# Optimization experiments

Measured on AMD Instinct MI355X. Metric: run time of the kernel, lower is better.

## Reference

```python
import jax, jax.numpy as jnp
import numpy as np

N = 50000          # nodes
E = 800000         # edges
IN = 256           # input feature dim
HID = 64           # hidden per-head dim
OUT = 64           # output dim
H1, H2 = 4, 1      # heads per layer
NEG_SLOPE = 0.2    # DGL GATConv default


def setup_inputs() -> dict:
    key = jax.random.key(0)
    ks = jax.random.split(key, 12)
    features = jax.random.normal(ks[0], (N, IN), dtype=jnp.float32)
    src = jax.random.randint(ks[1], (E,), 0, N, dtype=jnp.int32)
    dst = jax.random.randint(ks[2], (E,), 0, N, dtype=jnp.int32)
    s1 = 1.0 / np.sqrt(IN)
    s2 = 1.0 / np.sqrt(HID * H1)
    W1 = jax.random.normal(ks[3], (IN, H1 * HID), dtype=jnp.float32) * s1
    al1 = jax.random.normal(ks[4], (H1, HID), dtype=jnp.float32) * 0.1
    ar1 = jax.random.normal(ks[5], (H1, HID), dtype=jnp.float32) * 0.1
    b1 = jnp.zeros((H1, HID), dtype=jnp.float32)
    W2 = jax.random.normal(ks[6], (H1 * HID, H2 * OUT), dtype=jnp.float32) * s2
    al2 = jax.random.normal(ks[7], (H2, OUT), dtype=jnp.float32) * 0.1
    ar2 = jax.random.normal(ks[8], (H2, OUT), dtype=jnp.float32) * 0.1
    b2 = jnp.zeros((H2, OUT), dtype=jnp.float32)
    return {"features": features, "src": src, "dst": dst,
            "W1": W1, "al1": al1, "ar1": ar1, "b1": b1,
            "W2": W2, "al2": al2, "ar2": ar2, "b2": b2}


def gat_layer(h, src, dst, W, al, ar, b, heads, out_dim, activate):
    # projection: (N, H, D)
    feat = (h @ W).reshape(N, heads, out_dim)
    # per-node attention halves: (N, H)
    el = jnp.einsum('nhd,hd->nh', feat, al)
    er = jnp.einsum('nhd,hd->nh', feat, ar)
    # edge logits with leaky relu: (E, H)
    e = el[src] + er[dst]
    e = jnp.where(e >= 0, e, NEG_SLOPE * e)
    # edge softmax grouped by destination node
    emax = jax.ops.segment_max(e, dst, num_segments=N)      # (N, H)
    ee = jnp.exp(e - emax[dst])
    esum = jax.ops.segment_sum(ee, dst, num_segments=N)     # (N, H)
    alpha = ee / esum[dst]                                  # (E, H)
    # weighted scatter-sum of source features: (N, H, D)
    msg = alpha[:, :, None] * feat[src]
    out = jax.ops.segment_sum(msg, dst, num_segments=N) + b[None]
    if activate:
        out = jax.nn.relu(out)
    return out


def reference(features, src, dst, W1, al1, ar1, b1, W2, al2, ar2, b2):
    h = gat_layer(features, src, dst, W1, al1, ar1, b1, H1, HID, True)
    h = h.reshape(N, H1 * HID)                 # flatten(1)
    h = gat_layer(h, src, dst, W2, al2, ar2, b2, H2, OUT, False)
    return h.mean(axis=1)                      # mean over heads -> (N, OUT)
```

## Files before the change

### kernel.cpp

```cpp
#include <hip/hip_runtime.h>
#include <hip/hip_fp16.h>

#define NN   50000
#define NE   800000
#define IND  256
#define HIDD 64
#define OUTD 64
#define NH1  4
#define NH2  1
#define NEG  0.2f

#define NBUK 196
#define NCHK 256
#define CE   3125
#define MAXDEG 96

typedef float f32x4 __attribute__((ext_vector_type(4)));
typedef short s16x8 __attribute__((ext_vector_type(8)));

__device__ __forceinline__ short bf16_rne(float f) {
    unsigned u = __float_as_uint(f);
    unsigned r = u + 0x7FFFu + ((u >> 16) & 1u);
    return (short)(r >> 16);
}

__global__ void cnt1a_k(const int* __restrict__ key, int* __restrict__ cnt,
                        const float* __restrict__ W1, const float* __restrict__ W2,
                        short* __restrict__ Wt1, short* __restrict__ Wt2) {
    __shared__ int lc[NBUK];
    int tid = threadIdx.x, chunk = blockIdx.x;
    for (int idx = chunk * 256 + tid; idx < IND * IND + IND * OUTD; idx += NCHK * 256) {
        if (idx < IND * IND) {
            int k = idx / IND, n = idx - k * IND;
            Wt1[(size_t)n * IND + k] = bf16_rne(W1[idx]);
        } else {
            int i2 = idx - IND * IND;
            int k = i2 / OUTD, n = i2 - k * OUTD;
            Wt2[(size_t)n * IND + k] = bf16_rne(W2[i2]);
        }
    }
    for (int j = tid; j < NBUK; j += 256) lc[j] = 0;
    __syncthreads();
    const int* kc = key + (size_t)chunk * CE;
    for (int t = tid; t < CE; t += 256) atomicAdd(&lc[kc[t] >> 8], 1);
    __syncthreads();
    for (int j = tid; j < NBUK; j += 256) cnt[j * NCHK + chunk] = lc[j];
}

__global__ void cnt1b_k(const unsigned* __restrict__ ein, int* __restrict__ cnt) {
    __shared__ int lc[NBUK];
    int tid = threadIdx.x, chunk = blockIdx.x;
    for (int j = tid; j < NBUK; j += 256) lc[j] = 0;
    __syncthreads();
    const unsigned* ec = ein + (size_t)chunk * CE;
    for (int t = tid; t < CE; t += 256) atomicAdd(&lc[(ec[t] & 0xFFFFu) >> 8], 1);
    __syncthreads();
    for (int j = tid; j < NBUK; j += 256) cnt[j * NCHK + chunk] = lc[j];
}

__global__ void scanC_k(int* __restrict__ cnt, int* __restrict__ buktot) {
    int b    = blockIdx.x * 4 + (threadIdx.x >> 6);
    int lane = threadIdx.x & 63;
    if (b >= NBUK) return;
    int base = b * NCHK + lane * 4;
    int4 v = *(int4*)&cnt[base];
    int s0 = v.x, s1 = s0 + v.y, s2 = s1 + v.z, s3 = s2 + v.w;
    int inc = s3;
    for (int o = 1; o < 64; o <<= 1) {
        int t = __shfl_up(inc, o);
        if (lane >= o) inc += t;
    }
    int excl = inc - s3;
    int4 w;
    w.x = excl; w.y = excl + s0; w.z = excl + s1; w.w = excl + s2;
    *(int4*)&cnt[base] = w;
    if (lane == 63) buktot[b] = inc;
}

__global__ void fill1a_k(const int* __restrict__ src, const int* __restrict__ dst,
                         const int* __restrict__ cnt, const int* __restrict__ buktot,
                         unsigned* __restrict__ eout) {
    __shared__ int cur[NBUK];
    __shared__ int tmp[256];
    int tid = threadIdx.x, chunk = blockIdx.x;
    int v = (tid < NBUK) ? buktot[tid] : 0;
    tmp[tid] = v;
    __syncthreads();
    for (int o = 1; o < 256; o <<= 1) {
        int add = (tid >= o) ? tmp[tid - o] : 0;
        __syncthreads();
        tmp[tid] += add;
        __syncthreads();
    }
    if (tid < NBUK) cur[tid] = cnt[tid * NCHK + chunk] + tmp[tid] - v;
    __syncthreads();
    size_t base = (size_t)chunk * CE;
    for (int t = tid; t < CE; t += 256) {
        int s = src[base + t], d = dst[base + t];
        int pos = atomicAdd(&cur[s >> 8], 1);
        eout[pos] = ((unsigned)s << 16) | (unsigned)d;
    }
}

__global__ void fill1b_k(const unsigned* __restrict__ ein, const int* __restrict__ cnt,
                         const int* __restrict__ buktot, unsigned* __restrict__ eout) {
    __shared__ int cur[NBUK];
    __shared__ int tmp[256];
    int tid = threadIdx.x, chunk = blockIdx.x;
    int v = (tid < NBUK) ? buktot[tid] : 0;
    tmp[tid] = v;
    __syncthreads();
    for (int o = 1; o < 256; o <<= 1) {
        int add = (tid >= o) ? tmp[tid - o] : 0;
        __syncthreads();
        tmp[tid] += add;
        __syncthreads();
    }
    if (tid < NBUK) cur[tid] = cnt[tid * NCHK + chunk] + tmp[tid] - v;
    __syncthreads();
    const unsigned* ec = ein + (size_t)chunk * CE;
    for (int t = tid; t < CE; t += 256) {
        unsigned e = ec[t];
        int pos = atomicAdd(&cur[(e & 0xFFFFu) >> 8], 1);
        eout[pos] = e;
    }
}

__global__ void fill2_k(const unsigned* __restrict__ ein, const int* __restrict__ buktot,
                        int* __restrict__ off, int* __restrict__ deg,
                        int* __restrict__ src_sorted) {
    __shared__ int lh[256];
    __shared__ int tmp[256];
    __shared__ int cur[256];
    int tid = threadIdx.x, b = blockIdx.x;
    int v0 = (tid < NBUK) ? buktot[tid] : 0;
    tmp[tid] = v0;
    __syncthreads();
    for (int o = 1; o < 256; o <<= 1) {
        int add = (tid >= o) ? tmp[tid - o] : 0;
        __syncthreads();
        tmp[tid] += add;
        __syncthreads();
    }
    int beg = (b > 0) ? tmp[b - 1] : 0;
    int end = tmp[b];
    __syncthreads();
    int node0 = b << 8;
    lh[tid] = 0;
    __syncthreads();
    for (int e = beg + tid; e < end; e += 256)
        atomicAdd(&lh[(int)(ein[e] & 0xFFFFu) - node0], 1);
    __syncthreads();
    int v = lh[tid];
    tmp[tid] = v;
    __syncthreads();
    for (int o = 1; o < 256; o <<= 1) {
        int add = (tid >= o) ? tmp[tid - o] : 0;
        __syncthreads();
        tmp[tid] += add;
        __syncthreads();
    }
    int excl = tmp[tid] - v;
    int node = node0 + tid;
    if (node < NN) { deg[node] = v; off[node] = beg + excl; }
    cur[tid] = excl;
    __syncthreads();
    for (int e = beg + tid; e < end; e += 256) {
        unsigned ed = ein[e];
        int r = atomicAdd(&cur[(int)(ed & 0xFFFFu) - node0], 1);
        src_sorted[beg + r] = (int)(ed >> 16);
    }
}

__global__ __launch_bounds__(256) void gemm_l1(const float* __restrict__ A,
                                               const short* __restrict__ Bt,
                                               const float* __restrict__ al,
                                               const float* __restrict__ ar,
                                               __half* __restrict__ C,
                                               float* __restrict__ el,
                                               float* __restrict__ er, int M) {
    const int K = 256;
    __shared__ short As[64][40];
    __shared__ short Bs[256][40];

    int tid  = threadIdx.x;
    int wid  = tid >> 6, lane = tid & 63;
    int wm   = (wid >> 1) * 32;
    int wn   = (wid & 1) * 128;
    int row0 = blockIdx.x * 64;

    int arow = tid >> 2;
    int aseg = (tid & 3) * 8;
    int mr   = lane & 15;
    int kg   = (lane >> 4) * 8;

    f32x4 acc[2][8];
#pragma unroll
    for (int i = 0; i < 2; ++i)
#pragma unroll
        for (int j = 0; j < 8; ++j) acc[i][j] = (f32x4)(0.f);

    for (int k0 = 0; k0 < K; k0 += 32) {
        {
            int r = row0 + arow;
            float v[8];
            if (r < M) {
                float4 f0 = *(const float4*)&A[(size_t)r * K + k0 + aseg];
                float4 f1 = *(const float4*)&A[(size_t)r * K + k0 + aseg + 4];
                v[0] = f0.x; v[1] = f0.y; v[2] = f0.z; v[3] = f0.w;
                v[4] = f1.x; v[5] = f1.y; v[6] = f1.z; v[7] = f1.w;
            } else {
#pragma unroll
                for (int q = 0; q < 8; ++q) v[q] = 0.f;
            }
            short hi[8];
#pragma unroll
            for (int q = 0; q < 8; ++q) hi[q] = bf16_rne(v[q]);
            *(s16x8*)&As[arow][aseg] = *(s16x8*)&hi[0];
        }
        {
#pragma unroll
            for (int rep = 0; rep < 4; ++rep) {
                int n = rep * 64 + (tid >> 2);
                int ks = (tid & 3) * 8;
                *(s16x8*)&Bs[n][ks] = *(const s16x8*)&Bt[(size_t)n * K + k0 + ks];
            }
        }
        __syncthreads();

        s16x8 ah[2];
#pragma unroll
        for (int mi = 0; mi < 2; ++mi)
            ah[mi] = *(const s16x8*)&As[wm + mi * 16 + mr][kg];
#pragma unroll
        for (int ni = 0; ni < 8; ++ni) {
            s16x8 bhv = *(const s16x8*)&Bs[wn + ni * 16 + mr][kg];
#pragma unroll
            for (int mi = 0; mi < 2; ++mi)
                acc[mi][ni] = __builtin_amdgcn_mfma_f32_16x16x32_bf16(ah[mi], bhv, acc[mi][ni], 0, 0, 0);
        }
        __syncthreads();
    }

    float av[8], rv[8];
#pragma unroll
    for (int ni = 0; ni < 8; ++ni) {
        int c = wn + ni * 16 + mr;
        av[ni] = al[c];
        rv[ni] = ar[c];
    }
    int h0 = wn >> 6;

#pragma unroll
    for (int mi = 0; mi < 2; ++mi) {
#pragma unroll
        for (int r4 = 0; r4 < 4; ++r4) {
            int rr = row0 + wm + mi * 16 + (lane >> 4) * 4 + r4;
            if (rr < M) {
#pragma unroll
                for (int ni = 0; ni < 8; ++ni)
                    C[(size_t)rr * 256 + wn + ni * 16 + mr] = __float2half(acc[mi][ni][r4]);
            }
            float e0 = 0.f, e1 = 0.f, f0 = 0.f, f1 = 0.f;
#pragma unroll
            for (int ni = 0; ni < 4; ++ni) {
                e0 += acc[mi][ni][r4] * av[ni];
                f0 += acc[mi][ni][r4] * rv[ni];
            }
#pragma unroll
            for (int ni = 4; ni < 8; ++ni) {
                e1 += acc[mi][ni][r4] * av[ni];
                f1 += acc[mi][ni][r4] * rv[ni];
            }
#pragma unroll
            for (int o = 1; o <= 8; o <<= 1) {
                e0 += __shfl_xor(e0, o); e1 += __shfl_xor(e1, o);
                f0 += __shfl_xor(f0, o); f1 += __shfl_xor(f1, o);
            }
            if (mr == 0 && rr < M) {
                el[rr * 4 + h0]     = e0;
                el[rr * 4 + h0 + 1] = e1;
                er[rr * 4 + h0]     = f0;
                er[rr * 4 + h0 + 1] = f1;
            }
        }
    }
}

__global__ __launch_bounds__(256) void gemm_l2(const short* __restrict__ A,
                                               const short* __restrict__ Bt,
                                               const float* __restrict__ al,
                                               const float* __restrict__ ar,
                                               __half* __restrict__ C,
                                               float* __restrict__ el,
                                               float* __restrict__ er, int M) {
    const int K = 256;
    __shared__ short As[128][40];
    __shared__ short Bs[64][40];

    int tid  = threadIdx.x;
    int wid  = tid >> 6, lane = tid & 63;
    int wm   = wid * 32;
    int row0 = blockIdx.x * 128;

    int arow = tid >> 1;
    int aseg = (tid & 1) * 16;
    int mr   = lane & 15;
    int kg   = (lane >> 4) * 8;

    f32x4 acc[2][4];
#pragma unroll
    for (int i = 0; i < 2; ++i)
#pragma unroll
        for (int j = 0; j < 4; ++j) acc[i][j] = (f32x4)(0.f);

    for (int k0 = 0; k0 < K; k0 += 32) {
        {
            int r = row0 + arow;
            if (r < M) {
                *(s16x8*)&As[arow][aseg]     = *(const s16x8*)&A[(size_t)r * K + k0 + aseg];
                *(s16x8*)&As[arow][aseg + 8] = *(const s16x8*)&A[(size_t)r * K + k0 + aseg + 8];
            } else {
                s16x8 z = (s16x8)(short)0;
                *(s16x8*)&As[arow][aseg]     = z;
                *(s16x8*)&As[arow][aseg + 8] = z;
            }
        }
        {
            int n  = tid >> 2;
            int ks = (tid & 3) * 8;
            *(s16x8*)&Bs[n][ks] = *(const s16x8*)&Bt[(size_t)n * K + k0 + ks];
        }
        __syncthreads();

        s16x8 av_[2];
#pragma unroll
        for (int mi = 0; mi < 2; ++mi)
            av_[mi] = *(const s16x8*)&As[wm + mi * 16 + mr][kg];
#pragma unroll
        for (int ni = 0; ni < 4; ++ni) {
            s16x8 bhv = *(const s16x8*)&Bs[ni * 16 + mr][kg];
#pragma unroll
            for (int mi = 0; mi < 2; ++mi)
                acc[mi][ni] = __builtin_amdgcn_mfma_f32_16x16x32_bf16(av_[mi], bhv, acc[mi][ni], 0, 0, 0);
        }
        __syncthreads();
    }

    float av[4], rv[4];
#pragma unroll
    for (int ni = 0; ni < 4; ++ni) {
        int c = ni * 16 + mr;
        av[ni] = al[c];
        rv[ni] = ar[c];
    }

#pragma unroll
    for (int mi = 0; mi < 2; ++mi) {
#pragma unroll
        for (int r4 = 0; r4 < 4; ++r4) {
            int rr = row0 + wm + mi * 16 + (lane >> 4) * 4 + r4;
            if (rr < M) {
#pragma unroll
                for (int ni = 0; ni < 4; ++ni)
                    C[(size_t)rr * 64 + ni * 16 + mr] = __float2half(acc[mi][ni][r4]);
            }
            float e0 = 0.f, f0 = 0.f;
#pragma unroll
            for (int ni = 0; ni < 4; ++ni) {
                e0 += acc[mi][ni][r4] * av[ni];
                f0 += acc[mi][ni][r4] * rv[ni];
            }
#pragma unroll
            for (int o = 1; o <= 8; o <<= 1) {
                e0 += __shfl_xor(e0, o);
                f0 += __shfl_xor(f0, o);
            }
            if (mr == 0 && rr < M) { el[rr] = e0; er[rr] = f0; }
        }
    }
}

__global__ void agg_sm_l1(const __half* __restrict__ feat, const float* __restrict__ el,
                          const float* __restrict__ er, const int* __restrict__ src_sorted,
                          const int* __restrict__ off, const int* __restrict__ deg,
                          const float* __restrict__ bias, short* __restrict__ out) {
    __shared__ float alds[4][MAXDEG * 4];
    int w    = threadIdx.x >> 6;
    int wid  = blockIdx.x * 4 + w;
    int lane = threadIdx.x & 63;
    if (wid >= NN) return;
    int e   = lane >> 5;
    int c8  = (lane & 31) * 8;
    int h   = (lane & 31) >> 3;
    int k   = lane & 7;
    int sub = e * 8 + k;
    int beg = off[wid], dg = deg[wid];
    float erdh = er[(size_t)wid * 4 + h];

    float sum = 0.f;
    for (int p = sub; p < dg; p += 16) {
        int s = src_sorted[beg + p];
        float x = el[(size_t)s * 4 + h] + erdh;
        x = (x >= 0.f) ? x : NEG * x;
        float ex = __expf(x);
        if (p < MAXDEG) alds[w][p * 4 + h] = ex;
        sum += ex;
    }
    sum += __shfl_xor(sum, 1);
    sum += __shfl_xor(sum, 2);
    sum += __shfl_xor(sum, 4);
    sum += __shfl_xor(sum, 32);
    float inv = (dg > 0) ? 1.f / sum : 0.f;

    float acc[8] = {};
    int p = e;
    for (; p + 2 < dg; p += 4) {
        int s0 = src_sorted[beg + p];
        int s1 = src_sorted[beg + p + 2];
        float a0, a1;
        if (p < MAXDEG) a0 = alds[w][p * 4 + h];
        else {
            float x = el[(size_t)s0 * 4 + h] + erdh;
            x = (x >= 0.f) ? x : NEG * x;
            a0 = __expf(x);
        }
        if (p + 2 < MAXDEG) a1 = alds[w][(p + 2) * 4 + h];
        else {
            float x = el[(size_t)s1 * 4 + h] + erdh;
            x = (x >= 0.f) ? x : NEG * x;
            a1 = __expf(x);
        }
        float4 r0 = *(const float4*)&feat[(size_t)s0 * 256 + c8];
        float4 r1 = *(const float4*)&feat[(size_t)s1 * 256 + c8];
        __half2* h0 = (__half2*)&r0;
        __half2* h1 = (__half2*)&r1;
#pragma unroll
        for (int q = 0; q < 4; ++q) {
            float2 f0 = __half22float2(h0[q]);
            float2 f1 = __half22float2(h1[q]);
            acc[2 * q]     += a0 * f0.x + a1 * f1.x;
            acc[2 * q + 1] += a0 * f0.y + a1 * f1.y;
        }
    }
    for (; p < dg; p += 2) {
        int s = src_sorted[beg + p];
        float a;
        if (p < MAXDEG) a = alds[w][p * 4 + h];
        else {
            float x = el[(size_t)s * 4 + h] + erdh;
            x = (x >= 0.f) ? x : NEG * x;
            a = __expf(x);
        }
        float4 raw = *(const float4*)&feat[(size_t)s * 256 + c8];
        __half2* hh = (__half2*)&raw;
#pragma unroll
        for (int q = 0; q < 4; ++q) {
            float2 f = __half22float2(hh[q]);
            acc[2 * q]     += a * f.x;
            acc[2 * q + 1] += a * f.y;
        }
    }
#pragma unroll
    for (int q = 0; q < 8; ++q) acc[q] += __shfl_xor(acc[q], 32);
    if (e == 0) {
        short ob[8];
#pragma unroll
        for (int q = 0; q < 8; ++q) {
            float v = fmaxf(acc[q] * inv + bias[c8 + q], 0.f);
            ob[q] = bf16_rne(v);
        }
        *(s16x8*)&out[(size_t)wid * 256 + c8] = *(s16x8*)&ob[0];
    }
}

__global__ void agg_sm_l2(const __half* __restrict__ feat, const float* __restrict__ el,
                          const float* __restrict__ er, const int* __restrict__ src_sorted,
                          const int* __restrict__ off, const int* __restrict__ deg,
                          const float* __restrict__ bias, float* __restrict__ out) {
    __shared__ float alds[4][MAXDEG];
    int w    = threadIdx.x >> 6;
    int wid  = blockIdx.x * 4 + w;
    int lane = threadIdx.x & 63;
    if (wid >= NN) return;
    int e   = lane >> 3;
    int c8  = (lane & 7) * 8;
    int beg = off[wid], dg = deg[wid];
    float erd = er[wid];

    float sum = 0.f;
    for (int p = lane; p < dg; p += 64) {
        int s = src_sorted[beg + p];
        float x = el[s] + erd;
        x = (x >= 0.f) ? x : NEG * x;
        float ex = __expf(x);
        if (p < MAXDEG) alds[w][p] = ex;
        sum += ex;
    }
#pragma unroll
    for (int o = 1; o <= 32; o <<= 1) sum += __shfl_xor(sum, o);
    float inv = (dg > 0) ? 1.f / sum : 0.f;

    float acc[8] = {};
    for (int p = 0; p < dg; p += 8) {
        if (p + e < dg) {
            int s = src_sorted[beg + p + e];
            float a;
            if (p + e < MAXDEG) a = alds[w][p + e];
            else {
                float x = el[s] + erd;
                x = (x >= 0.f) ? x : NEG * x;
                a = __expf(x);
            }
            float4 raw = *(const float4*)&feat[(size_t)s * 64 + c8];
            __half2* hh = (__half2*)&raw;
#pragma unroll
            for (int q = 0; q < 4; ++q) {
                float2 f = __half22float2(hh[q]);
                acc[2 * q]     += a * f.x;
                acc[2 * q + 1] += a * f.y;
            }
        }
    }
#pragma unroll
    for (int o = 8; o <= 32; o <<= 1)
#pragma unroll
        for (int q = 0; q < 8; ++q) acc[q] += __shfl_xor(acc[q], o);
    if (e == 0) {
        float4 b0 = *(const float4*)&bias[c8];
        float4 b1 = *(const float4*)&bias[c8 + 4];
        float4 o0 = make_float4(acc[0] * inv + b0.x, acc[1] * inv + b0.y,
                                acc[2] * inv + b0.z, acc[3] * inv + b0.w);
        float4 o1 = make_float4(acc[4] * inv + b1.x, acc[5] * inv + b1.y,
                                acc[6] * inv + b1.z, acc[7] * inv + b1.w);
        *(float4*)&out[(size_t)wid * 64 + c8]     = o0;
        *(float4*)&out[(size_t)wid * 64 + c8 + 4] = o1;
    }
}

extern "C" void kernel_launch(void* const* d_in, const int* in_sizes, int n_in,
                              void* d_out, int out_size, void* d_ws, size_t ws_size,
                              hipStream_t stream) {
    const float* features = (const float*)d_in[0];
    const int*   src      = (const int*)  d_in[1];
    const int*   dst      = (const int*)  d_in[2];
    const float* W1       = (const float*)d_in[3];
    const float* al1      = (const float*)d_in[4];
    const float* ar1      = (const float*)d_in[5];
    const float* b1       = (const float*)d_in[6];
    const float* W2       = (const float*)d_in[7];
    const float* al2      = (const float*)d_in[8];
    const float* ar2      = (const float*)d_in[9];
    const float* b2       = (const float*)d_in[10];
    float* out = (float*)d_out;

    char* base = (char*)d_ws;
    size_t o = 0;
    __half* feat1h = (__half*)(base + o); o += (size_t)NN * 256 * 2;
    short*  h1b    = (short*) (base + o); o += (size_t)NN * 256 * 2;
    float*  el1 = (float*)(base + o); o += (size_t)NN * 4 * 4;
    float*  er1 = (float*)(base + o); o += (size_t)NN * 4 * 4;
    float*  el2 = (float*)(base + o); o += (size_t)NN * 4;
    float*  er2 = (float*)(base + o); o += (size_t)NN * 4;
    int* deg        = (int*)(base + o); o += (size_t)NN * 4;
    int* off        = (int*)(base + o); o += (size_t)NN * 4;
    int* src_sorted = (int*)(base + o); o += (size_t)NE * 4;
    int* cnt        = (int*)(base + o); o += (size_t)NBUK * NCHK * 4;
    int* buktot     = (int*)(base + o); o += 1024;
    unsigned* ebufS = (unsigned*)(base + o); o += (size_t)NE * 4;
    unsigned* ebufD = (unsigned*)(base + o); o += (size_t)NE * 4;
    short* Wt1 = (short*)(base + o); o += (size_t)IND * IND * 2;
    short* Wt2 = (short*)(base + o); o += (size_t)OUTD * IND * 2;

    __half* feat2h = feat1h;

    cnt1a_k<<<NCHK, 256, 0, stream>>>(src, cnt, W1, W2, Wt1, Wt2);
    scanC_k<<<(NBUK + 3) / 4, 256, 0, stream>>>(cnt, buktot);
    fill1a_k<<<NCHK, 256, 0, stream>>>(src, dst, cnt, buktot, ebufS);
    cnt1b_k<<<NCHK, 256, 0, stream>>>(ebufS, cnt);
    scanC_k<<<(NBUK + 3) / 4, 256, 0, stream>>>(cnt, buktot);
    fill1b_k<<<NCHK, 256, 0, stream>>>(ebufS, cnt, buktot, ebufD);
    fill2_k<<<NBUK, 256, 0, stream>>>(ebufD, buktot, off, deg, src_sorted);

    gemm_l1<<<(NN + 63) / 64, 256, 0, stream>>>(features, Wt1, al1, ar1,
                                                feat1h, el1, er1, NN);
    agg_sm_l1<<<(NN + 3) / 4, 256, 0, stream>>>(feat1h, el1, er1, src_sorted, off, deg,
                                                b1, h1b);

    gemm_l2<<<(NN + 127) / 128, 256, 0, stream>>>(h1b, Wt2, al2, ar2,
                                                  feat2h, el2, er2, NN);
    agg_sm_l2<<<(NN + 3) / 4, 256, 0, stream>>>(feat2h, el2, er2, src_sorted, off, deg,
                                                b2, out);
}
```

Baseline: 184.5 us.

## Replace two-pass radix sort with single dst bucketing plus LDS per-node insertion sort

The edge sort drops the first radix pass keyed by source and buckets edges by destination only. Within each destination bucket, fill2 scatters source ids into shared memory and each thread insertion-sorts its node's neighbor list, so source order within a segment is kept for locality. This removes one count/scan/fill kernel triple and an 800K-entry intermediate buffer. In exchange, fill2 gains serial per-thread insertion sorts and a large shared buffer that lowers occupancy, with a global fallback for buckets over 6144 edges.

```diff
diff --git a/kernel.cpp b/kernel.cpp
--- a/kernel.cpp
+++ b/kernel.cpp
@@ -14,6 +14,7 @@
 #define NCHK 256
 #define CE   3125
 #define MAXDEG 96
+#define SBUF 6144
 
 typedef float f32x4 __attribute__((ext_vector_type(4)));
 typedef short s16x8 __attribute__((ext_vector_type(8)));
@@ -24,9 +25,9 @@
     return (short)(r >> 16);
 }
 
-__global__ void cnt1a_k(const int* __restrict__ key, int* __restrict__ cnt,
-                        const float* __restrict__ W1, const float* __restrict__ W2,
-                        short* __restrict__ Wt1, short* __restrict__ Wt2) {
+__global__ void cnt1_k(const int* __restrict__ key, int* __restrict__ cnt,
+                       const float* __restrict__ W1, const float* __restrict__ W2,
+                       short* __restrict__ Wt1, short* __restrict__ Wt2) {
     __shared__ int lc[NBUK];
     int tid = threadIdx.x, chunk = blockIdx.x;
     for (int idx = chunk * 256 + tid; idx < IND * IND + IND * OUTD; idx += NCHK * 256) {
@@ -43,17 +44,6 @@
     __syncthreads();
     const int* kc = key + (size_t)chunk * CE;
     for (int t = tid; t < CE; t += 256) atomicAdd(&lc[kc[t] >> 8], 1);
-    __syncthreads();
-    for (int j = tid; j < NBUK; j += 256) cnt[j * NCHK + chunk] = lc[j];
-}
-
-__global__ void cnt1b_k(const unsigned* __restrict__ ein, int* __restrict__ cnt) {
-    __shared__ int lc[NBUK];
-    int tid = threadIdx.x, chunk = blockIdx.x;
-    for (int j = tid; j < NBUK; j += 256) lc[j] = 0;
-    __syncthreads();
-    const unsigned* ec = ein + (size_t)chunk * CE;
-    for (int t = tid; t < CE; t += 256) atomicAdd(&lc[(ec[t] & 0xFFFFu) >> 8], 1);
     __syncthreads();
     for (int j = tid; j < NBUK; j += 256) cnt[j * NCHK + chunk] = lc[j];
 }
@@ -77,9 +67,9 @@
     if (lane == 63) buktot[b] = inc;
 }
 
-__global__ void fill1a_k(const int* __restrict__ src, const int* __restrict__ dst,
-                         const int* __restrict__ cnt, const int* __restrict__ buktot,
-                         unsigned* __restrict__ eout) {
+__global__ void fill1_k(const int* __restrict__ src, const int* __restrict__ dst,
+                        const int* __restrict__ cnt, const int* __restrict__ buktot,
+                        unsigned* __restrict__ eout) {
     __shared__ int cur[NBUK];
     __shared__ int tmp[256];
     int tid = threadIdx.x, chunk = blockIdx.x;
@@ -97,32 +87,8 @@
     size_t base = (size_t)chunk * CE;
     for (int t = tid; t < CE; t += 256) {
         int s = src[base + t], d = dst[base + t];
-        int pos = atomicAdd(&cur[s >> 8], 1);
+        int pos = atomicAdd(&cur[d >> 8], 1);
         eout[pos] = ((unsigned)s << 16) | (unsigned)d;
-    }
-}
-
-__global__ void fill1b_k(const unsigned* __restrict__ ein, const int* __restrict__ cnt,
-                         const int* __restrict__ buktot, unsigned* __restrict__ eout) {
-    __shared__ int cur[NBUK];
-    __shared__ int tmp[256];
-    int tid = threadIdx.x, chunk = blockIdx.x;
-    int v = (tid < NBUK) ? buktot[tid] : 0;
-    tmp[tid] = v;
-    __syncthreads();
-    for (int o = 1; o < 256; o <<= 1) {
-        int add = (tid >= o) ? tmp[tid - o] : 0;
-        __syncthreads();
-        tmp[tid] += add;
-        __syncthreads();
-    }
-    if (tid < NBUK) cur[tid] = cnt[tid * NCHK + chunk] + tmp[tid] - v;
-    __syncthreads();
-    const unsigned* ec = ein + (size_t)chunk * CE;
-    for (int t = tid; t < CE; t += 256) {
-        unsigned e = ec[t];
-        int pos = atomicAdd(&cur[(e & 0xFFFFu) >> 8], 1);
-        eout[pos] = e;
     }
 }
 
@@ -132,6 +98,7 @@
     __shared__ int lh[256];
     __shared__ int tmp[256];
     __shared__ int cur[256];
+    __shared__ unsigned short sbuf[SBUF];
     int tid = threadIdx.x, b = blockIdx.x;
     int v0 = (tid < NBUK) ? buktot[tid] : 0;
     tmp[tid] = v0;
@@ -146,6 +113,7 @@
     int end = tmp[b];
     __syncthreads();
     int node0 = b << 8;
+    int nE = end - beg;
     lh[tid] = 0;
     __syncthreads();
     for (int e = beg + tid; e < end; e += 256)
@@ -165,10 +133,27 @@
     if (node < NN) { deg[node] = v; off[node] = beg + excl; }
     cur[tid] = excl;
     __syncthreads();
-    for (int e = beg + tid; e < end; e += 256) {
-        unsigned ed = ein[e];
-        int r = atomicAdd(&cur[(int)(ed & 0xFFFFu) - node0], 1);
-        src_sorted[beg + r] = (int)(ed >> 16);
+    if (nE <= SBUF) {
+        for (int e = beg + tid; e < end; e += 256) {
+            unsigned ed = ein[e];
+            int r = atomicAdd(&cur[(int)(ed & 0xFFFFu) - node0], 1);
+            sbuf[r] = (unsigned short)(ed >> 16);
+        }
+        __syncthreads();
+        for (int i = excl + 1; i < excl + v; ++i) {
+            unsigned short key = sbuf[i];
+            int j = i - 1;
+            while (j >= excl && sbuf[j] > key) { sbuf[j + 1] = sbuf[j]; --j; }
+            sbuf[j + 1] = key;
+        }
+        __syncthreads();
+        for (int e = tid; e < nE; e += 256) src_sorted[beg + e] = sbuf[e];
+    } else {
+        for (int e = beg + tid; e < end; e += 256) {
+            unsigned ed = ein[e];
+            int r = atomicAdd(&cur[(int)(ed & 0xFFFFu) - node0], 1);
+            src_sorted[beg + r] = (int)(ed >> 16);
+        }
     }
 }
 
@@ -567,19 +552,15 @@
     int* src_sorted = (int*)(base + o); o += (size_t)NE * 4;
     int* cnt        = (int*)(base + o); o += (size_t)NBUK * NCHK * 4;
     int* buktot     = (int*)(base + o); o += 1024;
-    unsigned* ebufS = (unsigned*)(base + o); o += (size_t)NE * 4;
     unsigned* ebufD = (unsigned*)(base + o); o += (size_t)NE * 4;
     short* Wt1 = (short*)(base + o); o += (size_t)IND * IND * 2;
     short* Wt2 = (short*)(base + o); o += (size_t)OUTD * IND * 2;
 
     __half* feat2h = feat1h;
 
-    cnt1a_k<<<NCHK, 256, 0, stream>>>(src, cnt, W1, W2, Wt1, Wt2);
+    cnt1_k <<<NCHK, 256, 0, stream>>>(dst, cnt, W1, W2, Wt1, Wt2);
     scanC_k<<<(NBUK + 3) / 4, 256, 0, stream>>>(cnt, buktot);
-    fill1a_k<<<NCHK, 256, 0, stream>>>(src, dst, cnt, buktot, ebufS);
-    cnt1b_k<<<NCHK, 256, 0, stream>>>(ebufS, cnt);
-    scanC_k<<<(NBUK + 3) / 4, 256, 0, stream>>>(cnt, buktot);
-    fill1b_k<<<NCHK, 256, 0, stream>>>(ebufS, cnt, buktot, ebufD);
+    fill1_k<<<NCHK, 256, 0, stream>>>(src, dst, cnt, buktot, ebufD);
     fill2_k<<<NBUK, 256, 0, stream>>>(ebufD, buktot, off, deg, src_sorted);
 
     gemm_l1<<<(NN + 63) / 64, 256, 0, stream>>>(features, Wt1, al1, ar1,
```

New measurement: 203.0 us. 1.1x slower.
